# Kernel tuning notes

Measured on AMD Instinct MI355X. Metric: run time of the kernel, lower is better.

Reference implementation:

```python
import jax, jax.numpy as jnp
import numpy as np

RANGES = (1, 2, 4, 10, 25)
B, L, D, V = 64, 1000, 300, 50000  # L divisible by every r in RANGES -> no remainder group


def setup_inputs() -> dict:
    key = jax.random.key(0)
    ks = jax.random.split(key, 12)
    u = lambda k, s: jax.random.uniform(k, s, dtype=jnp.float32) / 6  # matches torch.rand(...)/6
    return {
        "article_in": jax.random.randint(ks[0], (B, L), 0, V),
        "emb": jax.random.normal(ks[1], (V, D), dtype=jnp.float32) * 0.02,
        "w_ce": u(ks[2], (len(RANGES), D, D)),   # per-range W in contract-expand
        "b_ce": u(ks[3], (len(RANGES), 1, D)),   # per-range b (shape (1,D) in source)
        "w1": u(ks[4], (3, len(RANGES))),
        "b1": u(ks[5], (3, D)),
        "w2": u(ks[6], (1, 3)),
        "b2": u(ks[7], (1, D)),
        "wz": u(ks[8], (D, D)),
        "bz": u(ks[9], (1, D)),
        "wo": u(ks[10], (D, D)),
        "bo": u(ks[11], (1, D)),
    }


def _mru(x, w_ce, b_ce, w1, b1, w2, b2, wz, bz, wo, bo):
    b, l, d = x.shape
    # --- contract-expand: segment-sum windows of size r, tiny matmul, broadcast back /r ---
    ce = []
    for i, r in enumerate(RANGES):
        seg = x.reshape(b, l // r, r, d).sum(axis=2)                 # [B, L/r, D] segment sums
        t = jax.nn.relu(seg @ w_ce[i]) + b_ce[i]                     # relu(sum @ W) + b
        ce.append(jnp.repeat(t, r, axis=1) / r)                      # expand each group back, divided by r
    pre = jnp.stack(ce, axis=2)                                      # [B, L, 5, D]
    # --- multi-ranged reasoning MLP across the 5 ranges ---
    h1 = jax.nn.relu(jnp.einsum('ts,blsd->bltd', w1, pre) + b1)      # [B, L, 3, D]
    gate = jax.nn.relu(jnp.einsum('ot,bltd->blod', w2, h1) + b2)[:, :, 0, :]  # [B, L, D]
    # --- gated recurrent encoding (note: bias added OUTSIDE tanh, per source) ---
    z = jnp.tanh(x @ wz) + bz                                        # [B, L, D]
    o = jnp.tanh(x @ wo) + bo                                        # [B, L, D]

    def step(c, inp):
        g, zt, ot = inp
        c = g * c + (1.0 - g) * zt
        return c, ot * c

    seq = (gate.transpose(1, 0, 2), z.transpose(1, 0, 2), o.transpose(1, 0, 2))  # [L, B, D]
    _, h = jax.lax.scan(step, jnp.zeros((b, d), x.dtype), seq)
    return h.transpose(1, 0, 2)                                      # [B, L, D]


def reference(article_in, emb, w_ce, b_ce, w1, b1, w2, b2, wz, bz, wo, bo):
    x = emb[article_in]                                              # embedding lookup [B, L, D]
    return _mru(x, w_ce, b_ce, w1, b1, w2, b2, wz, bz, wo, bo)
```

## Files before the change

kernel.cpp:

```cpp
#include <hip/hip_runtime.h>
#include <hip/hip_bf16.h>

typedef unsigned short u16;
typedef unsigned int   u32;
typedef __attribute__((ext_vector_type(8))) short short8;
typedef __attribute__((ext_vector_type(4))) float floatx4;
typedef __attribute__((ext_vector_type(4))) unsigned short u16x4;

__device__ __forceinline__ u16 f2bf(float f){
  u32 x = __float_as_uint(f);
  u32 r = (x + 0x7fffu + ((x >> 16) & 1u)) >> 16;
  return (u16)r;
}
__device__ __forceinline__ float bf2f(u16 u){
  return __uint_as_float(((u32)u) << 16);
}
__device__ __forceinline__ float tanh_fast(float x){
  float xs = fminf(fmaxf(x, -16.f), 16.f);
  float e  = __builtin_amdgcn_exp2f(xs * 2.8853900817779268f);
  return (e - 1.f) * __builtin_amdgcn_rcpf(e + 1.f);
}
__device__ __forceinline__ void gload16(const void* g, void* l){
  __builtin_amdgcn_global_load_lds(
      (const __attribute__((address_space(1))) unsigned int*)g,
      (__attribute__((address_space(3))) unsigned int*)l, 16, 0, 0);
}

__global__ void k_gather_seg(const int* __restrict__ idx, const float* __restrict__ emb,
                             u16* __restrict__ x, u16* __restrict__ s2,
                             u16* __restrict__ s4, u16* __restrict__ s10, int total){
  int i = blockIdx.x * blockDim.x + threadIdx.x;
  if (i >= total) return;
  int d4 = i % 80; int rest = i / 80; int w = rest % 50; int b = rest / 50;
  const int dcol = d4 * 4;
  const int r0 = b * 1000 + w * 20;
  float a2[4] = {0,0,0,0}, a4[4] = {0,0,0,0}, a10[4] = {0,0,0,0};
  #pragma unroll
  for (int j = 0; j < 20; j++){
    const int r = r0 + j;
    u16x4 o; o[0] = 0; o[1] = 0; o[2] = 0; o[3] = 0;
    if (d4 < 75){
      const float4 v = *(const float4*)(emb + (size_t)idx[r] * 300 + dcol);
      o[0] = f2bf(v.x); o[1] = f2bf(v.y); o[2] = f2bf(v.z); o[3] = f2bf(v.w);
      a2[0] += v.x; a2[1] += v.y; a2[2] += v.z; a2[3] += v.w;
      a4[0] += v.x; a4[1] += v.y; a4[2] += v.z; a4[3] += v.w;
      a10[0] += v.x; a10[1] += v.y; a10[2] += v.z; a10[3] += v.w;
    }
    *(u16x4*)(x + (size_t)r * 320 + dcol) = o;
    if (j & 1){
      u16x4 s; 
      #pragma unroll
      for (int q = 0; q < 4; q++){ s[q] = f2bf(a2[q]); a2[q] = 0.f; }
      *(u16x4*)(s2 + ((size_t)(b * 500 + w * 10 + (j >> 1)) * 320 + dcol)) = s;
    }
    if ((j & 3) == 3){
      u16x4 s;
      #pragma unroll
      for (int q = 0; q < 4; q++){ s[q] = f2bf(a4[q]); a4[q] = 0.f; }
      *(u16x4*)(s4 + ((size_t)(b * 250 + w * 5 + (j >> 2)) * 320 + dcol)) = s;
    }
    if (j == 9 || j == 19){
      u16x4 s;
      #pragma unroll
      for (int q = 0; q < 4; q++){ s[q] = f2bf(a10[q]); a10[q] = 0.f; }
      *(u16x4*)(s10 + ((size_t)(b * 100 + w * 2 + j / 10) * 320 + dcol)) = s;
    }
  }
}

__global__ void k_s25(const u16* __restrict__ x, u16* __restrict__ s25, int total){
  int i = blockIdx.x * blockDim.x + threadIdx.x;
  if (i >= total) return;
  int d4 = i % 80; int rest = i / 80; int g = rest % 40; int b = rest / 40;
  const int dcol = d4 * 4;
  const u16* src = x + ((size_t)(b * 1000 + g * 25) * 320 + dcol);
  float a[4] = {0,0,0,0};
  #pragma unroll
  for (int j = 0; j < 25; j++){
    u16x4 v = *(const u16x4*)(src + (size_t)j * 320);
    #pragma unroll
    for (int q = 0; q < 4; q++) a[q] += bf2f(v[q]);
  }
  u16x4 o;
  #pragma unroll
  for (int q = 0; q < 4; q++) o[q] = f2bf(a[q]);
  *(u16x4*)(s25 + ((size_t)(b * 40 + g) * 320 + dcol)) = o;
}

__global__ void k_wprep(const float* __restrict__ wce, const float* __restrict__ wz,
                        const float* __restrict__ wo, u16* __restrict__ wT, int total){
  int i = blockIdx.x * blockDim.x + threadIdx.x;
  if (i >= total) return;
  int mat = i / 102400; int rem = i - mat * 102400;
  int n = rem / 320;    int k = rem - n * 320;
  float v = 0.f;
  if (n < 300 && k < 300){
    const float* src = (mat < 5) ? (wce + mat * 90000) : (mat == 5 ? wz : wo);
    v = src[k * 300 + n];
  }
  wT[i] = f2bf(v);
}

__global__ __launch_bounds__(256, 3) void k_gemm_all(
    const u16* __restrict__ x,  const u16* __restrict__ s2,
    const u16* __restrict__ s4, const u16* __restrict__ s10,
    const u16* __restrict__ s25,const u16* __restrict__ wT,
    u16* __restrict__ t0, u16* __restrict__ t1, u16* __restrict__ t2,
    u16* __restrict__ t3, u16* __restrict__ t4,
    u16* __restrict__ zb, u16* __restrict__ ob,
    const float* __restrict__ b_ce, const float* __restrict__ bz,
    const float* __restrict__ bo)
{
  __shared__ __align__(16) char lds[49152];

  const int bid = blockIdx.x;
  const u16 *A, *BT; u16* C; const float* bias;
  int mode; float scale; long tileRow;
  if (bid < 3000){
    const int xcd = bid & 7, j = bid >> 3;
    const int T = (j / 3) * 8 + xcd, m = j % 3;
    tileRow = (long)T * 64; A = x;
    if (m == 0)      { BT = wT;              C = t0; bias = b_ce; mode = 0; scale = 1.f; }
    else if (m == 1) { BT = wT + 5 * 102400; C = zb; bias = bz;   mode = 1; scale = 1.f; }
    else             { BT = wT + 6 * 102400; C = ob; bias = bo;   mode = 1; scale = 1.f; }
  } else {
    const int g = bid - 3000;
    if (g < 500)      { A=s2;  BT=wT+1*102400; C=t1; bias=b_ce+300;  mode=0; scale=0.5f;  tileRow=(long)g*64; }
    else if (g < 750) { A=s4;  BT=wT+2*102400; C=t2; bias=b_ce+600;  mode=0; scale=0.25f; tileRow=(long)(g-500)*64; }
    else if (g < 850) { A=s10; BT=wT+3*102400; C=t3; bias=b_ce+900;  mode=0; scale=0.1f;  tileRow=(long)(g-750)*64; }
    else              { A=s25; BT=wT+4*102400; C=t4; bias=b_ce+1200; mode=0; scale=0.04f; tileRow=(long)(g-850)*64; }
  }

  const int tid  = threadIdx.x;
  const int lane = tid & 63;
  const int wid  = tid >> 6;

  const int arow = tid >> 2, ac = tid & 3;
  const u16* aSrc = A + (tileRow + arow) * 320 + ((ac ^ ((arow >> 1) & 3)) << 3);
  const u16* bSrc[5];
  #pragma unroll
  for (int l = 0; l < 5; l++){
    const int idx2 = l * 256 + tid, col = idx2 >> 2, cc = idx2 & 3;
    bSrc[l] = BT + col * 320 + ((cc ^ ((col >> 1) & 3)) << 3);
  }
  const int wbase = wid * 1024;

  const int rA  = lane & 15;
  const int cBt = wid * 80 + (lane & 15);
  const int kchunk = ((lane >> 4) ^ ((lane >> 1) & 3)) << 4;

  floatx4 acc[4][5];
  #pragma unroll
  for (int m = 0; m < 4; m++)
    #pragma unroll
    for (int n = 0; n < 5; n++)
      #pragma unroll
      for (int q = 0; q < 4; q++) acc[m][n][q] = 0.f;

  gload16(aSrc, lds + wbase);
  #pragma unroll
  for (int l = 0; l < 5; l++) gload16(bSrc[l], lds + 8192 + l * 4096 + wbase);
  __syncthreads();

  #pragma unroll
  for (int t = 0; t < 10; t++){
    const int cur = t & 1;
    if (t < 9){
      const int nb = cur ^ 1;
      gload16(aSrc + (t + 1) * 32, lds + nb * 4096 + wbase);
      #pragma unroll
      for (int l = 0; l < 5; l++)
        gload16(bSrc[l] + (t + 1) * 32, lds + 8192 + nb * 20480 + l * 4096 + wbase);
    }
    const char* bA = lds + cur * 4096;
    const char* bB = lds + 8192 + cur * 20480;
    short8 af[4], bf[5];
    #pragma unroll
    for (int m = 0; m < 4; m++)
      af[m] = *(const short8*)(bA + (rA + m * 16) * 64 + kchunk);
    #pragma unroll
    for (int n = 0; n < 5; n++)
      bf[n] = *(const short8*)(bB + (cBt + n * 16) * 64 + kchunk);
    #pragma unroll
    for (int m = 0; m < 4; m++)
      #pragma unroll
      for (int n = 0; n < 5; n++)
        acc[m][n] = __builtin_amdgcn_mfma_f32_16x16x32_bf16(af[m], bf[n], acc[m][n], 0, 0, 0);
    __syncthreads();
  }

  const int colbase = wid * 80 + (lane & 15);
  const long rowb   = tileRow + ((lane >> 4) << 2);
  #pragma unroll
  for (int m = 0; m < 4; m++){
    #pragma unroll
    for (int n = 0; n < 5; n++){
      const int gcol = colbase + n * 16;
      if (gcol < 300){
        const float bv = bias[gcol];
        #pragma unroll
        for (int r = 0; r < 4; r++){
          const long grow = rowb + m * 16 + r;
          float v = acc[m][n][r];
          v = (mode == 0) ? (fmaxf(v, 0.f) + bv) * scale : tanh_fast(v) + bv;
          C[grow * 300 + gcol] = f2bf(v);
        }
      }
    }
  }
}

__device__ __forceinline__ float gate_eval(
    float p0, float p1, float p2, float p3, float p4,
    const float W1[3][5], const float W2[3], const float B1[3], float B2)
{
  float acc2 = B2;
  #pragma unroll
  for (int t = 0; t < 3; t++){
    float u = W1[t][0]*p0 + W1[t][1]*p1 + W1[t][2]*p2 + W1[t][3]*p3 + W1[t][4]*p4 + B1[t];
    acc2 += W2[t] * fmaxf(u, 0.f);
  }
  return fmaxf(acc2, 0.f);
}

__global__ void k_scan1(const u16* __restrict__ t0, const u16* __restrict__ t1,
    const u16* __restrict__ t2, const u16* __restrict__ t3, const u16* __restrict__ t4,
    const u16* __restrict__ z,
    const float* __restrict__ w1, const float* __restrict__ b1,
    const float* __restrict__ w2, const float* __restrict__ b2,
    float* __restrict__ cA, float* __restrict__ cB, int total)
{
  int i = blockIdx.x * blockDim.x + threadIdx.x;
  if (i >= total) return;
  int d4 = i % 75; int rest = i / 75; int ch = rest % 40; int b = rest / 40;
  const int d = d4 * 4;
  float W1[3][5], W2[3], B1[3][4], B2[4];
  #pragma unroll
  for (int t = 0; t < 3; t++){
    #pragma unroll
    for (int s = 0; s < 5; s++) W1[t][s] = w1[t * 5 + s];
    W2[t] = w2[t];
    #pragma unroll
    for (int q = 0; q < 4; q++) B1[t][q] = b1[t * 300 + d + q];
  }
  #pragma unroll
  for (int q = 0; q < 4; q++) B2[q] = b2[d + q];
  float Ac[4] = {1.f,1.f,1.f,1.f}, Bc[4] = {0.f,0.f,0.f,0.f};
  const int l0 = ch * 25;
  const u16x4 v4 = *(const u16x4*)(t4 + (size_t)(b * 40 + ch) * 300 + d);
  for (int l = l0; l < l0 + 25; l++){
    u16x4 v0 = *(const u16x4*)(t0 + (size_t)(b * 1000 + l)        * 300 + d);
    u16x4 v1 = *(const u16x4*)(t1 + (size_t)(b * 500  + (l >> 1)) * 300 + d);
    u16x4 v2 = *(const u16x4*)(t2 + (size_t)(b * 250  + (l >> 2)) * 300 + d);
    u16x4 v3 = *(const u16x4*)(t3 + (size_t)(b * 100  + l / 10)   * 300 + d);
    u16x4 vz = *(const u16x4*)(z  + (size_t)(b * 1000 + l)        * 300 + d);
    #pragma unroll
    for (int q = 0; q < 4; q++){
      float B1q[3] = {B1[0][q], B1[1][q], B1[2][q]};
      float g  = gate_eval(bf2f(v0[q]), bf2f(v1[q]), bf2f(v2[q]), bf2f(v3[q]), bf2f(v4[q]),
                           W1, W2, B1q, B2[q]);
      Ac[q] = g * Ac[q];
      Bc[q] = g * Bc[q] + (1.f - g) * bf2f(vz[q]);
    }
  }
  *(float4*)(cA + (size_t)ch * 19200 + b * 300 + d) = make_float4(Ac[0], Ac[1], Ac[2], Ac[3]);
  *(float4*)(cB + (size_t)ch * 19200 + b * 300 + d) = make_float4(Bc[0], Bc[1], Bc[2], Bc[3]);
}

__global__ void k_scan2(const float* __restrict__ cA, const float* __restrict__ cB,
                        float* __restrict__ cinit, int total){
  int i = blockIdx.x * blockDim.x + threadIdx.x;
  if (i >= total) return;
  float c = 0.f;
  for (int ch = 0; ch < 40; ch++){
    cinit[ch * 19200 + i] = c;
    c = cA[ch * 19200 + i] * c + cB[ch * 19200 + i];
  }
}

__global__ void k_scan3(const u16* __restrict__ t0, const u16* __restrict__ t1,
    const u16* __restrict__ t2, const u16* __restrict__ t3, const u16* __restrict__ t4,
    const u16* __restrict__ z, const u16* __restrict__ o,
    const float* __restrict__ cinit,
    const float* __restrict__ w1, const float* __restrict__ b1,
    const float* __restrict__ w2, const float* __restrict__ b2,
    float* __restrict__ out, int total)
{
  int i = blockIdx.x * blockDim.x + threadIdx.x;
  if (i >= total) return;
  int d4 = i % 75; int rest = i / 75; int ch = rest % 40; int b = rest / 40;
  const int d = d4 * 4;
  float W1[3][5], W2[3], B1[3][4], B2[4];
  #pragma unroll
  for (int t = 0; t < 3; t++){
    #pragma unroll
    for (int s = 0; s < 5; s++) W1[t][s] = w1[t * 5 + s];
    W2[t] = w2[t];
    #pragma unroll
    for (int q = 0; q < 4; q++) B1[t][q] = b1[t * 300 + d + q];
  }
  #pragma unroll
  for (int q = 0; q < 4; q++) B2[q] = b2[d + q];
  float c[4];
  {
    float4 ci = *(const float4*)(cinit + (size_t)ch * 19200 + b * 300 + d);
    c[0] = ci.x; c[1] = ci.y; c[2] = ci.z; c[3] = ci.w;
  }
  const int l0 = ch * 25;
  const u16x4 v4 = *(const u16x4*)(t4 + (size_t)(b * 40 + ch) * 300 + d);
  for (int l = l0; l < l0 + 25; l++){
    u16x4 v0 = *(const u16x4*)(t0 + (size_t)(b * 1000 + l)        * 300 + d);
    u16x4 v1 = *(const u16x4*)(t1 + (size_t)(b * 500  + (l >> 1)) * 300 + d);
    u16x4 v2 = *(const u16x4*)(t2 + (size_t)(b * 250  + (l >> 2)) * 300 + d);
    u16x4 v3 = *(const u16x4*)(t3 + (size_t)(b * 100  + l / 10)   * 300 + d);
    u16x4 vz = *(const u16x4*)(z  + (size_t)(b * 1000 + l)        * 300 + d);
    u16x4 vo = *(const u16x4*)(o  + (size_t)(b * 1000 + l)        * 300 + d);
    float4 res;
    #pragma unroll
    for (int q = 0; q < 4; q++){
      float B1q[3] = {B1[0][q], B1[1][q], B1[2][q]};
      float g  = gate_eval(bf2f(v0[q]), bf2f(v1[q]), bf2f(v2[q]), bf2f(v3[q]), bf2f(v4[q]),
                           W1, W2, B1q, B2[q]);
      c[q] = g * c[q] + (1.f - g) * bf2f(vz[q]);
      ((float*)&res)[q] = bf2f(vo[q]) * c[q];
    }
    *(float4*)(out + (size_t)(b * 1000 + l) * 300 + d) = res;
  }
}

extern "C" void kernel_launch(void* const* d_in, const int* in_sizes, int n_in,
                              void* d_out, int out_size, void* d_ws, size_t ws_size,
                              hipStream_t stream){
  const int*   article = (const int*)  d_in[0];
  const float* emb     = (const float*)d_in[1];
  const float* w_ce    = (const float*)d_in[2];
  const float* b_ce    = (const float*)d_in[3];
  const float* w1      = (const float*)d_in[4];
  const float* b1      = (const float*)d_in[5];
  const float* w2      = (const float*)d_in[6];
  const float* b2      = (const float*)d_in[7];
  const float* wz      = (const float*)d_in[8];
  const float* bz      = (const float*)d_in[9];
  const float* wo      = (const float*)d_in[10];
  const float* bo      = (const float*)d_in[11];
  float* out = (float*)d_out;
  char*  ws  = (char*)d_ws;

  u16* x    = (u16*)(ws + 0UL);
  u16* s2   = (u16*)(ws + 40960000UL);
  u16* s4   = (u16*)(ws + 61440000UL);
  u16* s10  = (u16*)(ws + 71680000UL);
  u16* s25  = (u16*)(ws + 75776000UL);
  u16* wT   = (u16*)(ws + 77414400UL);
  u16* t0   = (u16*)(ws + 78848000UL);
  u16* t1   = (u16*)(ws + 117248000UL);
  u16* t2   = (u16*)(ws + 136448000UL);
  u16* t3   = (u16*)(ws + 146048000UL);
  u16* t4   = (u16*)(ws + 149888000UL);
  u16* zb   = (u16*)(ws + 151424000UL);
  u16* ob   = (u16*)(ws + 189824000UL);
  float* cA = (float*)(ws + 40960000UL);
  float* cB = (float*)(ws + 44032000UL);
  float* ci = (float*)(ws + 47104000UL);
  (void)ws_size; (void)in_sizes; (void)n_in; (void)out_size;

  k_wprep     <<<2800, 256, 0, stream>>>(w_ce, wz, wo, wT, 716800);
  k_gather_seg<<<1000, 256, 0, stream>>>(article, emb, x, s2, s4, s10, 256000);
  k_s25       <<< 800, 256, 0, stream>>>(x, s25, 204800);

  k_gemm_all<<<3890, 256, 0, stream>>>(x, s2, s4, s10, s25, wT,
                                       t0, t1, t2, t3, t4, zb, ob,
                                       b_ce, bz, bo);

  k_scan1<<<750, 256, 0, stream>>>(t0, t1, t2, t3, t4, zb, w1, b1, w2, b2, cA, cB, 192000);
  k_scan2<<< 75, 256, 0, stream>>>(cA, cB, ci, 19200);
  k_scan3<<<750, 256, 0, stream>>>(t0, t1, t2, t3, t4, zb, ob, ci, w1, b1, w2, b2, out, 192000);
}
```

Before: 240.8 us.

## Retile fused GEMM to 256x160 blocks with 2x2 wave layout

Changes the batched GEMM tile from 64 rows x 320 columns per block to 256 rows x 160 columns, with four waves arranged 2x2 and each computing 128x80. Each B tile is now reused across four times as many rows, and the grid drops from 3890 to 1982 blocks, which is meant to cut global and LDS traffic per MFMA. The cost is a larger accumulator (8x5 floatx4 per wave), occupancy lowered to 2 blocks per CU, and row-bounds checks for the partial tiles of the segment GEMMs. Part of the B tile load is issued by only half the threads.

```diff
diff --git a/kernel.cpp b/kernel.cpp
--- a/kernel.cpp
+++ b/kernel.cpp
@@ -48,7 +48,7 @@
     }
     *(u16x4*)(x + (size_t)r * 320 + dcol) = o;
     if (j & 1){
-      u16x4 s; 
+      u16x4 s;
       #pragma unroll
       for (int q = 0; q < 4; q++){ s[q] = f2bf(a2[q]); a2[q] = 0.f; }
       *(u16x4*)(s2 + ((size_t)(b * 500 + w * 10 + (j >> 1)) * 320 + dcol)) = s;
@@ -101,7 +101,7 @@
   wT[i] = f2bf(v);
 }
 
-__global__ __launch_bounds__(256, 3) void k_gemm_all(
+__global__ __launch_bounds__(256, 2) void k_gemm_all(
     const u16* __restrict__ x,  const u16* __restrict__ s2,
     const u16* __restrict__ s4, const u16* __restrict__ s10,
     const u16* __restrict__ s25,const u16* __restrict__ wT,
@@ -111,99 +111,117 @@
     const float* __restrict__ b_ce, const float* __restrict__ bz,
     const float* __restrict__ bo)
 {
-  __shared__ __align__(16) char lds[49152];
+  __shared__ __align__(16) char lds[53248];
 
   const int bid = blockIdx.x;
   const u16 *A, *BT; u16* C; const float* bias;
-  int mode; float scale; long tileRow;
-  if (bid < 3000){
-    const int xcd = bid & 7, j = bid >> 3;
-    const int T = (j / 3) * 8 + xcd, m = j % 3;
-    tileRow = (long)T * 64; A = x;
-    if (m == 0)      { BT = wT;              C = t0; bias = b_ce; mode = 0; scale = 1.f; }
-    else if (m == 1) { BT = wT + 5 * 102400; C = zb; bias = bz;   mode = 1; scale = 1.f; }
-    else             { BT = wT + 6 * 102400; C = ob; bias = bo;   mode = 1; scale = 1.f; }
+  int mode; float scale; long tileRow, Mrows; int colBase;
+  if (bid < 1536){
+    const int xcd = bid & 7, r = bid >> 3;
+    const int g = r / 6, within = r % 6;
+    const int stripe = g * 8 + xcd;
+    if (stripe >= 250) return;
+    const int mat = within >> 1; colBase = (within & 1) * 160;
+    tileRow = (long)stripe * 256; A = x; Mrows = 64000;
+    if (mat == 0)      { BT = wT;              C = t0; bias = b_ce; mode = 0; scale = 1.f; }
+    else if (mat == 1) { BT = wT + 5 * 102400; C = zb; bias = bz;   mode = 1; scale = 1.f; }
+    else               { BT = wT + 6 * 102400; C = ob; bias = bo;   mode = 1; scale = 1.f; }
   } else {
-    const int g = bid - 3000;
-    if (g < 500)      { A=s2;  BT=wT+1*102400; C=t1; bias=b_ce+300;  mode=0; scale=0.5f;  tileRow=(long)g*64; }
-    else if (g < 750) { A=s4;  BT=wT+2*102400; C=t2; bias=b_ce+600;  mode=0; scale=0.25f; tileRow=(long)(g-500)*64; }
-    else if (g < 850) { A=s10; BT=wT+3*102400; C=t3; bias=b_ce+900;  mode=0; scale=0.1f;  tileRow=(long)(g-750)*64; }
-    else              { A=s25; BT=wT+4*102400; C=t4; bias=b_ce+1200; mode=0; scale=0.04f; tileRow=(long)(g-850)*64; }
+    const int g2 = bid - 1536;
+    int h;
+    if (g2 < 250)      { h = g2;       A=s2;  BT=wT+1*102400; C=t1; bias=b_ce+300;  mode=0; scale=0.5f;  Mrows=32000; }
+    else if (g2 < 376) { h = g2 - 250; A=s4;  BT=wT+2*102400; C=t2; bias=b_ce+600;  mode=0; scale=0.25f; Mrows=16000; }
+    else if (g2 < 426) { h = g2 - 376; A=s10; BT=wT+3*102400; C=t3; bias=b_ce+900;  mode=0; scale=0.1f;  Mrows=6400; }
+    else               { h = g2 - 426; A=s25; BT=wT+4*102400; C=t4; bias=b_ce+1200; mode=0; scale=0.04f; Mrows=2560; }
+    tileRow = (long)(h >> 1) * 256; colBase = (h & 1) * 160;
   }
 
   const int tid  = threadIdx.x;
   const int lane = tid & 63;
   const int wid  = tid >> 6;
-
-  const int arow = tid >> 2, ac = tid & 3;
-  const u16* aSrc = A + (tileRow + arow) * 320 + ((ac ^ ((arow >> 1) & 3)) << 3);
-  const u16* bSrc[5];
-  #pragma unroll
-  for (int l = 0; l < 5; l++){
-    const int idx2 = l * 256 + tid, col = idx2 >> 2, cc = idx2 & 3;
-    bSrc[l] = BT + col * 320 + ((cc ^ ((col >> 1) & 3)) << 3);
-  }
-  const int wbase = wid * 1024;
-
-  const int rA  = lane & 15;
-  const int cBt = wid * 80 + (lane & 15);
-  const int kchunk = ((lane >> 4) ^ ((lane >> 1) & 3)) << 4;
-
-  floatx4 acc[4][5];
-  #pragma unroll
-  for (int m = 0; m < 4; m++)
+  const int wr   = wid >> 1;
+  const int wc   = wid & 1;
+  const int L    = lane & 15;
+  const int kc   = lane >> 4;
+
+  const u16* aS[4];
+  #pragma unroll
+  for (int l = 0; l < 4; l++){
+    const int idx = l * 256 + tid, row = idx >> 2, c = idx & 3;
+    aS[l] = A + (tileRow + row) * 320 + ((c ^ ((row >> 1) & 3)) << 3);
+  }
+  const u16* bS[3];
+  #pragma unroll
+  for (int l = 0; l < 3; l++){
+    const int idx = l * 256 + tid;
+    const int brow = idx >> 3, ps = idx & 7, pos = ps ^ (brow & 7);
+    const int col = colBase + brow * 2 + (pos >> 2), kcc = pos & 3;
+    bS[l] = BT + col * 320 + kcc * 8;
+  }
+
+  const int aR    = wr * 128 + L;
+  const int aBase = aR * 64 + ((kc ^ ((aR >> 1) & 3)) << 4);
+  const int rb    = wc * 40 + (L >> 1);
+  const int bBase = rb * 128 + (((((L & 1) << 2) | kc) ^ (rb & 7)) << 4);
+
+  floatx4 acc[8][5];
+  #pragma unroll
+  for (int m = 0; m < 8; m++)
     #pragma unroll
     for (int n = 0; n < 5; n++)
       #pragma unroll
       for (int q = 0; q < 4; q++) acc[m][n][q] = 0.f;
 
-  gload16(aSrc, lds + wbase);
-  #pragma unroll
-  for (int l = 0; l < 5; l++) gload16(bSrc[l], lds + 8192 + l * 4096 + wbase);
+  #define STAGE(t, nb) do {                                                     \
+    _Pragma("unroll")                                                           \
+    for (int l = 0; l < 4; l++)                                                 \
+      gload16(aS[l] + (t) * 32, lds + (nb) * 16384 + (l * 256 + wid * 64) * 16);\
+    _Pragma("unroll")                                                           \
+    for (int l = 0; l < 2; l++)                                                 \
+      gload16(bS[l] + (t) * 32, lds + 32768 + (nb) * 10240 + (l * 256 + wid * 64) * 16); \
+    if (tid < 128)                                                              \
+      gload16(bS[2] + (t) * 32, lds + 32768 + (nb) * 10240 + (512 + wid * 64) * 16); \
+  } while (0)
+
+  STAGE(0, 0);
   __syncthreads();
 
   #pragma unroll
   for (int t = 0; t < 10; t++){
     const int cur = t & 1;
-    if (t < 9){
-      const int nb = cur ^ 1;
-      gload16(aSrc + (t + 1) * 32, lds + nb * 4096 + wbase);
-      #pragma unroll
-      for (int l = 0; l < 5; l++)
-        gload16(bSrc[l] + (t + 1) * 32, lds + 8192 + nb * 20480 + l * 4096 + wbase);
-    }
-    const char* bA = lds + cur * 4096;
-    const char* bB = lds + 8192 + cur * 20480;
-    short8 af[4], bf[5];
-    #pragma unroll
-    for (int m = 0; m < 4; m++)
-      af[m] = *(const short8*)(bA + (rA + m * 16) * 64 + kchunk);
-    #pragma unroll
-    for (int n = 0; n < 5; n++)
-      bf[n] = *(const short8*)(bB + (cBt + n * 16) * 64 + kchunk);
-    #pragma unroll
-    for (int m = 0; m < 4; m++)
+    if (t < 9) STAGE(t + 1, cur ^ 1);
+    const char* Ab = lds + cur * 16384;
+    const char* Bb = lds + 32768 + cur * 10240;
+    short8 af[8], bf[5];
+    #pragma unroll
+    for (int m = 0; m < 8; m++) af[m] = *(const short8*)(Ab + aBase + m * 1024);
+    #pragma unroll
+    for (int n = 0; n < 5; n++) bf[n] = *(const short8*)(Bb + bBase + n * 1024);
+    #pragma unroll
+    for (int m = 0; m < 8; m++)
       #pragma unroll
       for (int n = 0; n < 5; n++)
         acc[m][n] = __builtin_amdgcn_mfma_f32_16x16x32_bf16(af[m], bf[n], acc[m][n], 0, 0, 0);
     __syncthreads();
   }
-
-  const int colbase = wid * 80 + (lane & 15);
-  const long rowb   = tileRow + ((lane >> 4) << 2);
-  #pragma unroll
-  for (int m = 0; m < 4; m++){
-    #pragma unroll
-    for (int n = 0; n < 5; n++){
-      const int gcol = colbase + n * 16;
-      if (gcol < 300){
-        const float bv = bias[gcol];
+  #undef STAGE
+
+  const long rowb = tileRow + wr * 128 + (kc << 2);
+  #pragma unroll
+  for (int n = 0; n < 5; n++){
+    const int gcol = colBase + wc * 80 + n * 16 + L;
+    if (gcol < 300){
+      const float bv = bias[gcol];
+      #pragma unroll
+      for (int m = 0; m < 8; m++){
         #pragma unroll
-        for (int r = 0; r < 4; r++){
-          const long grow = rowb + m * 16 + r;
-          float v = acc[m][n][r];
-          v = (mode == 0) ? (fmaxf(v, 0.f) + bv) * scale : tanh_fast(v) + bv;
-          C[grow * 300 + gcol] = f2bf(v);
+        for (int r2 = 0; r2 < 4; r2++){
+          const long grow = rowb + m * 16 + r2;
+          if (grow < Mrows){
+            float v = acc[m][n][r2];
+            v = (mode == 0) ? (fmaxf(v, 0.f) + bv) * scale : tanh_fast(v) + bv;
+            C[grow * 300 + gcol] = f2bf(v);
+          }
         }
       }
     }
@@ -368,7 +386,7 @@
   k_gather_seg<<<1000, 256, 0, stream>>>(article, emb, x, s2, s4, s10, 256000);
   k_s25       <<< 800, 256, 0, stream>>>(x, s25, 204800);
 
-  k_gemm_all<<<3890, 256, 0, stream>>>(x, s2, s4, s10, s25, wT,
+  k_gemm_all<<<1982, 256, 0, stream>>>(x, s2, s4, s10, s25, wT,
                                        t0, t1, t2, t3, t4, zb, ob,
                                        b_ce, bz, bo);
 
```

Measured after the change: 353.6 us. 46.8% more time.

## Triple-buffer GEMM K-loop with explicit vmcnt waits and single barrier

Applied to the files above, without the earlier changes.

Replaces the double-buffered LDS pipeline in the fused GEMM kernel with a three-stage ring, prefetching two K-steps ahead. Each iteration waits on outstanding global-to-LDS loads with a partial s_waitcnt and uses one barrier instead of two syncs, so loads overlap more with MFMA work. In exchange LDS grows to 72KB per block and launch bounds drop from 3 to 2 blocks per CU, which lowers occupancy.

```diff
diff --git a/kernel.cpp b/kernel.cpp
--- a/kernel.cpp
+++ b/kernel.cpp
@@ -48,7 +48,7 @@
     }
     *(u16x4*)(x + (size_t)r * 320 + dcol) = o;
     if (j & 1){
-      u16x4 s; 
+      u16x4 s;
       #pragma unroll
       for (int q = 0; q < 4; q++){ s[q] = f2bf(a2[q]); a2[q] = 0.f; }
       *(u16x4*)(s2 + ((size_t)(b * 500 + w * 10 + (j >> 1)) * 320 + dcol)) = s;
@@ -101,7 +101,7 @@
   wT[i] = f2bf(v);
 }
 
-__global__ __launch_bounds__(256, 3) void k_gemm_all(
+__global__ __launch_bounds__(256, 2) void k_gemm_all(
     const u16* __restrict__ x,  const u16* __restrict__ s2,
     const u16* __restrict__ s4, const u16* __restrict__ s10,
     const u16* __restrict__ s25,const u16* __restrict__ wT,
@@ -111,7 +111,7 @@
     const float* __restrict__ b_ce, const float* __restrict__ bz,
     const float* __restrict__ bo)
 {
-  __shared__ __align__(16) char lds[49152];
+  __shared__ __align__(16) char lds[73728];
 
   const int bid = blockIdx.x;
   const u16 *A, *BT; u16* C; const float* bias;
@@ -157,37 +157,39 @@
       #pragma unroll
       for (int q = 0; q < 4; q++) acc[m][n][q] = 0.f;
 
-  gload16(aSrc, lds + wbase);
-  #pragma unroll
-  for (int l = 0; l < 5; l++) gload16(bSrc[l], lds + 8192 + l * 4096 + wbase);
-  __syncthreads();
+  #define STAGE(t, nb) do {                                                   \
+    gload16(aSrc + (t) * 32, lds + (nb) * 24576 + wbase);                     \
+    _Pragma("unroll")                                                         \
+    for (int l = 0; l < 5; l++)                                               \
+      gload16(bSrc[l] + (t) * 32, lds + (nb) * 24576 + 4096 + l * 4096 + wbase); \
+  } while (0)
+
+  STAGE(0, 0);
+  STAGE(1, 1);
 
   #pragma unroll
   for (int t = 0; t < 10; t++){
-    const int cur = t & 1;
-    if (t < 9){
-      const int nb = cur ^ 1;
-      gload16(aSrc + (t + 1) * 32, lds + nb * 4096 + wbase);
-      #pragma unroll
-      for (int l = 0; l < 5; l++)
-        gload16(bSrc[l] + (t + 1) * 32, lds + 8192 + nb * 20480 + l * 4096 + wbase);
-    }
-    const char* bA = lds + cur * 4096;
-    const char* bB = lds + 8192 + cur * 20480;
+    if (t < 9) asm volatile("s_waitcnt vmcnt(6)" ::: "memory");
+    else       asm volatile("s_waitcnt vmcnt(0)" ::: "memory");
+    __builtin_amdgcn_s_barrier();
+    __builtin_amdgcn_sched_barrier(0);
+    if (t < 8) STAGE(t + 2, (t + 2) % 3);
+    const char* Ab = lds + (t % 3) * 24576;
+    const char* Bb = Ab + 4096;
     short8 af[4], bf[5];
     #pragma unroll
     for (int m = 0; m < 4; m++)
-      af[m] = *(const short8*)(bA + (rA + m * 16) * 64 + kchunk);
+      af[m] = *(const short8*)(Ab + (rA + m * 16) * 64 + kchunk);
     #pragma unroll
     for (int n = 0; n < 5; n++)
-      bf[n] = *(const short8*)(bB + (cBt + n * 16) * 64 + kchunk);
+      bf[n] = *(const short8*)(Bb + (cBt + n * 16) * 64 + kchunk);
     #pragma unroll
     for (int m = 0; m < 4; m++)
       #pragma unroll
       for (int n = 0; n < 5; n++)
         acc[m][n] = __builtin_amdgcn_mfma_f32_16x16x32_bf16(af[m], bf[n], acc[m][n], 0, 0, 0);
-    __syncthreads();
-  }
+  }
+  #undef STAGE
 
   const int colbase = wid * 80 + (lane & 15);
   const long rowb   = tileRow + ((lane >> 4) << 2);
```

Result: slower. 287.2 us (+19.2%).

## Make GEMM persistent with LDS-resident weight slice and direct-register A loads

Applied to the files above, without the earlier changes.

The batched GEMM becomes a persistent kernel of 768 blocks, each walking a contiguous range of work items. Each item is a 256-row by 80-column tile. The block keeps an 80-column slice of the weight matrix resident in LDS, reloading it only when the matrix or column group changes. A operands are loaded straight from global memory into registers with a one-step prefetch instead of being staged through double-buffered LDS. This is meant to cut repeated weight traffic, per-K-step barriers and launch tail effects. The cost is uncoalesced 16-byte A loads, more register pressure, and load imbalance from the range-based partitioning.

```diff
diff --git a/kernel.cpp b/kernel.cpp
--- a/kernel.cpp
+++ b/kernel.cpp
@@ -48,7 +48,7 @@
     }
     *(u16x4*)(x + (size_t)r * 320 + dcol) = o;
     if (j & 1){
-      u16x4 s; 
+      u16x4 s;
       #pragma unroll
       for (int q = 0; q < 4; q++){ s[q] = f2bf(a2[q]); a2[q] = 0.f; }
       *(u16x4*)(s2 + ((size_t)(b * 500 + w * 10 + (j >> 1)) * 320 + dcol)) = s;
@@ -111,99 +111,107 @@
     const float* __restrict__ b_ce, const float* __restrict__ bz,
     const float* __restrict__ bo)
 {
-  __shared__ __align__(16) char lds[49152];
-
-  const int bid = blockIdx.x;
-  const u16 *A, *BT; u16* C; const float* bias;
-  int mode; float scale; long tileRow;
-  if (bid < 3000){
-    const int xcd = bid & 7, j = bid >> 3;
-    const int T = (j / 3) * 8 + xcd, m = j % 3;
-    tileRow = (long)T * 64; A = x;
-    if (m == 0)      { BT = wT;              C = t0; bias = b_ce; mode = 0; scale = 1.f; }
-    else if (m == 1) { BT = wT + 5 * 102400; C = zb; bias = bz;   mode = 1; scale = 1.f; }
-    else             { BT = wT + 6 * 102400; C = ob; bias = bo;   mode = 1; scale = 1.f; }
-  } else {
-    const int g = bid - 3000;
-    if (g < 500)      { A=s2;  BT=wT+1*102400; C=t1; bias=b_ce+300;  mode=0; scale=0.5f;  tileRow=(long)g*64; }
-    else if (g < 750) { A=s4;  BT=wT+2*102400; C=t2; bias=b_ce+600;  mode=0; scale=0.25f; tileRow=(long)(g-500)*64; }
-    else if (g < 850) { A=s10; BT=wT+3*102400; C=t3; bias=b_ce+900;  mode=0; scale=0.1f;  tileRow=(long)(g-750)*64; }
-    else              { A=s25; BT=wT+4*102400; C=t4; bias=b_ce+1200; mode=0; scale=0.04f; tileRow=(long)(g-850)*64; }
-  }
-
+  __shared__ __align__(16) u16 W[25600];
+
+  const int bid  = blockIdx.x;
+  const int j0   = (int)(((long)bid * 3892) / 768);
+  const int j1   = (int)(((long)(bid + 1) * 3892) / 768);
   const int tid  = threadIdx.x;
   const int lane = tid & 63;
   const int wid  = tid >> 6;
-
-  const int arow = tid >> 2, ac = tid & 3;
-  const u16* aSrc = A + (tileRow + arow) * 320 + ((ac ^ ((arow >> 1) & 3)) << 3);
-  const u16* bSrc[5];
-  #pragma unroll
-  for (int l = 0; l < 5; l++){
-    const int idx2 = l * 256 + tid, col = idx2 >> 2, cc = idx2 & 3;
-    bSrc[l] = BT + col * 320 + ((cc ^ ((col >> 1) & 3)) << 3);
-  }
-  const int wbase = wid * 1024;
-
-  const int rA  = lane & 15;
-  const int cBt = wid * 80 + (lane & 15);
-  const int kchunk = ((lane >> 4) ^ ((lane >> 1) & 3)) << 4;
-
-  floatx4 acc[4][5];
-  #pragma unroll
-  for (int m = 0; m < 4; m++)
-    #pragma unroll
-    for (int n = 0; n < 5; n++)
-      #pragma unroll
-      for (int q = 0; q < 4; q++) acc[m][n][q] = 0.f;
-
-  gload16(aSrc, lds + wbase);
-  #pragma unroll
-  for (int l = 0; l < 5; l++) gload16(bSrc[l], lds + 8192 + l * 4096 + wbase);
-  __syncthreads();
-
-  #pragma unroll
-  for (int t = 0; t < 10; t++){
-    const int cur = t & 1;
-    if (t < 9){
-      const int nb = cur ^ 1;
-      gload16(aSrc + (t + 1) * 32, lds + nb * 4096 + wbase);
-      #pragma unroll
-      for (int l = 0; l < 5; l++)
-        gload16(bSrc[l] + (t + 1) * 32, lds + 8192 + nb * 20480 + l * 4096 + wbase);
-    }
-    const char* bA = lds + cur * 4096;
-    const char* bB = lds + 8192 + cur * 20480;
-    short8 af[4], bf[5];
+  const int L    = lane & 15;
+  const int kc   = lane >> 4;
+
+  int curGroup = -1;
+
+  for (int j = j0; j < j1; ++j){
+    int mat, q, r;
+    if (j < 3000){ mat = j / 1000; int lo = j - mat * 1000; q = lo / 250; r = lo - q * 250; }
+    else if (j < 3500){ mat = 3; int lo = j - 3000; q = lo / 125; r = lo - q * 125; }
+    else if (j < 3752){ mat = 4; int lo = j - 3500; q = lo / 63;  r = lo - q * 63; }
+    else if (j < 3852){ mat = 5; int lo = j - 3752; q = lo / 25;  r = lo - q * 25; }
+    else              { mat = 6; int lo = j - 3852; q = lo / 10;  r = lo - q * 10; }
+
+    const u16* A; u16* C; const float* bias; int mode; float scale; long Mrows; int wOff;
+    switch (mat){
+      case 0:  A = x;   C = t0; bias = b_ce;       mode = 0; scale = 1.f;   Mrows = 64000; wOff = 0; break;
+      case 1:  A = x;   C = zb; bias = bz;         mode = 1; scale = 1.f;   Mrows = 64000; wOff = 5; break;
+      case 2:  A = x;   C = ob; bias = bo;         mode = 1; scale = 1.f;   Mrows = 64000; wOff = 6; break;
+      case 3:  A = s2;  C = t1; bias = b_ce + 300; mode = 0; scale = 0.5f;  Mrows = 32000; wOff = 1; break;
+      case 4:  A = s4;  C = t2; bias = b_ce + 600; mode = 0; scale = 0.25f; Mrows = 16000; wOff = 2; break;
+      case 5:  A = s10; C = t3; bias = b_ce + 900; mode = 0; scale = 0.1f;  Mrows = 6400;  wOff = 3; break;
+      default: A = s25; C = t4; bias = b_ce + 1200;mode = 0; scale = 0.04f; Mrows = 2560;  wOff = 4; break;
+    }
+
+    const int grp = mat * 4 + q;
+    if (grp != curGroup){
+      curGroup = grp;
+      __syncthreads();
+      const u16* Wq = wT + wOff * 102400 + q * 80 * 320;
+      #pragma unroll
+      for (int i = 0; i < 13; i++){
+        const int c = i * 256 + tid;
+        if (c < 3200){
+          const int col = c / 40, p = c - col * 40;
+          const int s = (p & ~7) | ((p & 7) ^ (col & 7));
+          gload16(Wq + col * 320 + s * 8, (char*)W + (i * 256 + wid * 64) * 16);
+        }
+      }
+      __syncthreads();
+    }
+
+    const long rowBase = (long)r * 256 + wid * 64;
+    const u16* aP = A + (rowBase + L) * 320 + kc * 8;
+
+    floatx4 acc[4][5];
     #pragma unroll
     for (int m = 0; m < 4; m++)
-      af[m] = *(const short8*)(bA + (rA + m * 16) * 64 + kchunk);
-    #pragma unroll
-    for (int n = 0; n < 5; n++)
-      bf[n] = *(const short8*)(bB + (cBt + n * 16) * 64 + kchunk);
-    #pragma unroll
-    for (int m = 0; m < 4; m++)
       #pragma unroll
       for (int n = 0; n < 5; n++)
-        acc[m][n] = __builtin_amdgcn_mfma_f32_16x16x32_bf16(af[m], bf[n], acc[m][n], 0, 0, 0);
-    __syncthreads();
-  }
-
-  const int colbase = wid * 80 + (lane & 15);
-  const long rowb   = tileRow + ((lane >> 4) << 2);
-  #pragma unroll
-  for (int m = 0; m < 4; m++){
+        #pragma unroll
+        for (int z2 = 0; z2 < 4; z2++) acc[m][n][z2] = 0.f;
+
+    short8 ca[4], na[4];
+    #pragma unroll
+    for (int m = 0; m < 4; m++) ca[m] = *(const short8*)(aP + m * 16 * 320);
+
+    #pragma unroll
+    for (int t = 0; t < 10; t++){
+      if (t < 9){
+        #pragma unroll
+        for (int m = 0; m < 4; m++)
+          na[m] = *(const short8*)(aP + m * 16 * 320 + (t + 1) * 32);
+      }
+      short8 bf[5];
+      #pragma unroll
+      for (int n = 0; n < 5; n++)
+        bf[n] = *(const short8*)((const char*)W + (n * 16 + L) * 640 + (t >> 1) * 128
+                                 + (((4 * (t & 1) + kc) ^ (L & 7)) << 4));
+      #pragma unroll
+      for (int m = 0; m < 4; m++)
+        #pragma unroll
+        for (int n = 0; n < 5; n++)
+          acc[m][n] = __builtin_amdgcn_mfma_f32_16x16x32_bf16(ca[m], bf[n], acc[m][n], 0, 0, 0);
+      #pragma unroll
+      for (int m = 0; m < 4; m++) ca[m] = na[m];
+    }
+
     #pragma unroll
     for (int n = 0; n < 5; n++){
-      const int gcol = colbase + n * 16;
+      const int gcol = q * 80 + n * 16 + L;
       if (gcol < 300){
         const float bv = bias[gcol];
         #pragma unroll
-        for (int r = 0; r < 4; r++){
-          const long grow = rowb + m * 16 + r;
-          float v = acc[m][n][r];
-          v = (mode == 0) ? (fmaxf(v, 0.f) + bv) * scale : tanh_fast(v) + bv;
-          C[grow * 300 + gcol] = f2bf(v);
+        for (int m = 0; m < 4; m++){
+          #pragma unroll
+          for (int reg = 0; reg < 4; reg++){
+            const long grow = rowBase + m * 16 + kc * 4 + reg;
+            if (grow < Mrows){
+              float v = acc[m][n][reg];
+              v = (mode == 0) ? (fmaxf(v, 0.f) + bv) * scale : tanh_fast(v) + bv;
+              C[grow * 300 + gcol] = f2bf(v);
+            }
+          }
         }
       }
     }
@@ -368,9 +376,9 @@
   k_gather_seg<<<1000, 256, 0, stream>>>(article, emb, x, s2, s4, s10, 256000);
   k_s25       <<< 800, 256, 0, stream>>>(x, s25, 204800);
 
-  k_gemm_all<<<3890, 256, 0, stream>>>(x, s2, s4, s10, s25, wT,
-                                       t0, t1, t2, t3, t4, zb, ob,
-                                       b_ce, bz, bo);
+  k_gemm_all<<<768, 256, 0, stream>>>(x, s2, s4, s10, s25, wT,
+                                      t0, t1, t2, t3, t4, zb, ob,
+                                      b_ce, bz, bo);
 
   k_scan1<<<750, 256, 0, stream>>>(t0, t1, t2, t3, t4, zb, w1, b1, w2, b2, cA, cB, 192000);
   k_scan2<<< 75, 256, 0, stream>>>(cA, cB, ci, 19200);
```

New measurement: 383.9 us. 59.4% more time.
